# Performance work log

Hardware: AMD Instinct MI355X
Metric: run time of the kernel (lower is better)

## Reference

```python
import jax, jax.numpy as jnp
import numpy as np

DELTA = 5.0          # weight on positive BCE term
R = 0.01             # hard-negative fraction
M, N = 4096, 16384   # batch rows, memory-bank size
NUM_HARD = int(R * (N - 1))  # int(r * neg_count); each row has exactly 1 positive


def setup_inputs() -> dict:
    key = jax.random.key(0)
    k1, k2 = jax.random.split(key)
    inputs = jax.random.normal(k1, (M, N), dtype=jnp.float32)
    targets = jax.random.randint(k2, (M,), 0, N)
    return {"inputs": inputs, "targets": targets}


def reference(inputs, targets):
    m, n = inputs.shape
    rows = jnp.arange(m)
    # positive logit per row (one-hot scatter => exactly one positive)
    pos = inputs[rows, targets]                          # [m]
    # BCE with logits, target=1: softplus(-x); mean over the single positive
    l_pos = jax.nn.softplus(-pos)                        # [m]
    # exclude positive from negatives by sinking it to -inf, then hard top-k
    neg_inf = jnp.finfo(inputs.dtype).min
    masked = inputs.at[rows, targets].set(neg_inf)       # [m, n]
    hard_neg, _ = jax.lax.top_k(masked, NUM_HARD)        # [m, NUM_HARD]
    # BCE with logits, target=0: softplus(x); mean over hard negatives
    l_neg = jnp.mean(jax.nn.softplus(hard_neg), axis=1)  # [m]
    return jnp.mean(DELTA * l_pos + l_neg)
```

## Files before the change

kernel.cpp:

```cpp
#include <hip/hip_runtime.h>
#include <stdint.h>

#define M_ROWS 4096
#define N_COLS 16384
#define K_HARD 163
#define DELTA_W 5.0f
#define CAP    1024
#define NB1    4096
#define NB2    1024
#define BLOCK  256

__device__ __forceinline__ uint32_t f2key(float x) {
    uint32_t u = __float_as_uint(x);
    return u ^ (((int32_t)u >> 31) | 0x80000000u);
}
__device__ __forceinline__ float key2f(uint32_t k) {
    uint32_t u = (k & 0x80000000u) ? (k & 0x7fffffffu) : ~k;
    return __uint_as_float(u);
}
__device__ __forceinline__ float softplus_f(float x) {
    return fmaxf(x, 0.0f) + log1pf(__expf(-fabsf(x)));
}

#define KEY_MIN 0xC0000000u

__device__ void pivot_scan(const uint32_t* hist, int nb, int K,
                           int* part, int* pivot, int* krem) {
    const int t = threadIdx.x;
    const int bpt = nb / BLOCK;
    const int base = t * bpt;
    int mypart = 0;
    for (int i = 0; i < bpt; ++i) mypart += (int)hist[base + i];
    part[t] = mypart;
    __syncthreads();
    for (int off = 1; off < BLOCK; off <<= 1) {
        int v = part[t];
        if (t + off < BLOCK) v += part[t + off];
        __syncthreads();
        part[t] = v;
        __syncthreads();
    }
    const int above = part[t] - mypart;
    if (above < K && above + mypart >= K) {
        int running = above;
        for (int b = base + bpt - 1; b >= base; --b) {
            int c = (int)hist[b];
            if (running < K && running + c >= K) { *pivot = b; *krem = K - running; }
            running += c;
        }
    }
    __syncthreads();
}

__global__ __launch_bounds__(BLOCK) void mmcl_kernel(
        const float* __restrict__ inputs,
        const int* __restrict__ targets,
        float* __restrict__ out) {
    __shared__ uint32_t s_hist[NB1];
    __shared__ uint32_t s_cand[CAP];
    __shared__ int s_part[BLOCK];
    __shared__ int s_ncand;
    __shared__ int s_found;
    __shared__ int s_pivot;
    __shared__ int s_krem;
    __shared__ float s_pos;
    __shared__ float s_wsum[BLOCK / 64];

    const int row = blockIdx.x;
    const int t = threadIdx.x;
    const int lane = t & 63;
    const float* rowp = inputs + (size_t)row * N_COLS;
    const int target = targets[row];

    for (int i = t; i < NB1; i += BLOCK) s_hist[i] = 0;
    if (t == 0) { s_ncand = 0; s_found = -1; s_pos = rowp[target]; }
    __syncthreads();

    const float4* rp4 = (const float4*)rowp;
#pragma unroll 4
    for (int it = 0; it < N_COLS / (BLOCK * 4); ++it) {
        const float4 v = rp4[it * BLOCK + t];
        const uint32_t k0 = f2key(v.x), k1 = f2key(v.y),
                       k2 = f2key(v.z), k3 = f2key(v.w);
        if (k0 >= KEY_MIN) { int i = atomicAdd(&s_ncand, 1); if (i < CAP) s_cand[i] = k0; }
        if (k1 >= KEY_MIN) { int i = atomicAdd(&s_ncand, 1); if (i < CAP) s_cand[i] = k1; }
        if (k2 >= KEY_MIN) { int i = atomicAdd(&s_ncand, 1); if (i < CAP) s_cand[i] = k2; }
        if (k3 >= KEY_MIN) { int i = atomicAdd(&s_ncand, 1); if (i < CAP) s_cand[i] = k3; }
    }
    __syncthreads();

    const int ncand_raw = s_ncand;
    const uint32_t tkey = f2key(s_pos);
    const bool no_ovf = (ncand_raw <= CAP);
    if (no_ovf && tkey >= KEY_MIN) {
        for (int i = t; i < ncand_raw; i += BLOCK)
            if (s_cand[i] == tkey) { atomicCAS(&s_found, -1, i); break; }
    }
    __syncthreads();
    if (t == 0 && s_found >= 0) {
        s_cand[s_found] = s_cand[ncand_raw - 1];
        s_ncand = ncand_raw - 1;
    }
    __syncthreads();
    const int ncand = s_ncand;
    const bool fast = no_ovf && (ncand >= K_HARD);

    float local = 0.0f;
    uint32_t T;
    int tie;

    if (fast) {
        for (int i = t; i < ncand; i += BLOCK)
            atomicAdd(&s_hist[s_cand[i] >> 20], 1u);
        __syncthreads();
        pivot_scan(s_hist, NB1, K_HARD, s_part, &s_pivot, &s_krem);
        const int p1 = s_pivot, k1r = s_krem;

        for (int i = t; i < NB2; i += BLOCK) s_hist[i] = 0;
        __syncthreads();
        for (int i = t; i < ncand; i += BLOCK) {
            const uint32_t k = s_cand[i];
            if ((int)(k >> 20) == p1) atomicAdd(&s_hist[(k >> 10) & 1023u], 1u);
        }
        __syncthreads();
        pivot_scan(s_hist, NB2, k1r, s_part, &s_pivot, &s_krem);
        const int p2 = s_pivot, k2r = s_krem;
        const uint32_t pref2 = ((uint32_t)p1 << 10) | (uint32_t)p2;

        for (int i = t; i < NB2; i += BLOCK) s_hist[i] = 0;
        __syncthreads();
        for (int i = t; i < ncand; i += BLOCK) {
            const uint32_t k = s_cand[i];
            if ((k >> 10) == pref2) atomicAdd(&s_hist[k & 1023u], 1u);
        }
        __syncthreads();
        pivot_scan(s_hist, NB2, k2r, s_part, &s_pivot, &s_krem);
        T = (pref2 << 10) | (uint32_t)s_pivot;
        tie = s_krem;

        for (int i = t; i < ncand; i += BLOCK) {
            const uint32_t k = s_cand[i];
            if (k > T) local += softplus_f(key2f(k));
        }
    } else {
        for (int i = t; i < NB1; i += BLOCK) s_hist[i] = 0;
        __syncthreads();
        for (int j = t; j < N_COLS; j += BLOCK) {
            if (j == target) continue;
            atomicAdd(&s_hist[f2key(rowp[j]) >> 20], 1u);
        }
        __syncthreads();
        pivot_scan(s_hist, NB1, K_HARD, s_part, &s_pivot, &s_krem);
        const int p1 = s_pivot, k1r = s_krem;

        for (int i = t; i < NB2; i += BLOCK) s_hist[i] = 0;
        __syncthreads();
        for (int j = t; j < N_COLS; j += BLOCK) {
            if (j == target) continue;
            const uint32_t k = f2key(rowp[j]);
            if ((int)(k >> 20) == p1) atomicAdd(&s_hist[(k >> 10) & 1023u], 1u);
        }
        __syncthreads();
        pivot_scan(s_hist, NB2, k1r, s_part, &s_pivot, &s_krem);
        const int p2 = s_pivot, k2r = s_krem;
        const uint32_t pref2 = ((uint32_t)p1 << 10) | (uint32_t)p2;

        for (int i = t; i < NB2; i += BLOCK) s_hist[i] = 0;
        __syncthreads();
        for (int j = t; j < N_COLS; j += BLOCK) {
            if (j == target) continue;
            const uint32_t k = f2key(rowp[j]);
            if ((k >> 10) == pref2) atomicAdd(&s_hist[k & 1023u], 1u);
        }
        __syncthreads();
        pivot_scan(s_hist, NB2, k2r, s_part, &s_pivot, &s_krem);
        T = (pref2 << 10) | (uint32_t)s_pivot;
        tie = s_krem;

        for (int j = t; j < N_COLS; j += BLOCK) {
            if (j == target) continue;
            const uint32_t k = f2key(rowp[j]);
            if (k > T) local += softplus_f(key2f(k));
        }
    }

    for (int off = 32; off > 0; off >>= 1) local += __shfl_down(local, off);
    if (lane == 0) s_wsum[t >> 6] = local;
    __syncthreads();
    if (t == 0) {
        float tot = 0.0f;
        for (int w = 0; w < BLOCK / 64; ++w) tot += s_wsum[w];
        tot += (float)tie * softplus_f(key2f(T));
        const float l_neg = tot / (float)K_HARD;
        const float l_pos = softplus_f(-s_pos);
        const float rowval = (DELTA_W * l_pos + l_neg) * (1.0f / (float)M_ROWS);
        atomicAdd(out, rowval);
    }
}

__global__ void mmcl_zero_out(float* out) { out[0] = 0.0f; }

extern "C" void kernel_launch(void* const* d_in, const int* in_sizes, int n_in,
                              void* d_out, int out_size, void* d_ws, size_t ws_size,
                              hipStream_t stream) {
    const float* inputs = (const float*)d_in[0];
    const int* targets = (const int*)d_in[1];
    float* out = (float*)d_out;
    mmcl_zero_out<<<1, 1, 0, stream>>>(out);
    mmcl_kernel<<<M_ROWS, BLOCK, 0, stream>>>(inputs, targets, out);
}
```

Measured before the change: 400.3 us.

## Process eight rows per 1024-thread block with wave-level candidate selection

Replaces the one-row-per-256-thread-block kernel with 1024-thread blocks that stream eight rows each. Candidates at or above a fixed threshold of 2.0 are compacted into per-wave shared segments with a ballot/shuffle prefix sum, which removes the shared-memory atomic counter. Each row's radix select then runs inside a single wave using shuffle-based scans with no block barriers. A deterministic two-kernel partial-sum reduction replaces the global atomicAdd and the zeroing kernel. The risk is that the fixed threshold and the 64-entry segment cap push rows into the slow single-wave full-row fallback more often, and only half the waves take part in the selection phase.

```diff
diff --git a/kernel.cpp b/kernel.cpp
--- a/kernel.cpp
+++ b/kernel.cpp
@@ -5,14 +5,17 @@
 #define N_COLS 16384
 #define K_HARD 163
 #define DELTA_W 5.0f
-#define CAP    1024
-#define NB1    4096
-#define NB2    1024
-#define BLOCK  256
+#define THREADS 1024
+#define NWAVES  16
+#define RPB     8
+#define GRID    (M_ROWS / RPB)
+#define THRESH  2.0f
+#define KEY_MIN 0xC0000000u
+#define SEGC    64
 
 __device__ __forceinline__ uint32_t f2key(float x) {
     uint32_t u = __float_as_uint(x);
-    return u ^ (((int32_t)u >> 31) | 0x80000000u);
+    return u ^ (uint32_t)(((int32_t)u >> 31) | 0x80000000u);
 }
 __device__ __forceinline__ float key2f(uint32_t k) {
     uint32_t u = (k & 0x80000000u) ? (k & 0x7fffffffu) : ~k;
@@ -22,183 +25,224 @@
     return fmaxf(x, 0.0f) + log1pf(__expf(-fabsf(x)));
 }
 
-#define KEY_MIN 0xC0000000u
-
-__device__ void pivot_scan(const uint32_t* hist, int nb, int K,
-                           int* part, int* pivot, int* krem) {
-    const int t = threadIdx.x;
-    const int bpt = nb / BLOCK;
-    const int base = t * bpt;
-    int mypart = 0;
-    for (int i = 0; i < bpt; ++i) mypart += (int)hist[base + i];
-    part[t] = mypart;
-    __syncthreads();
-    for (int off = 1; off < BLOCK; off <<= 1) {
-        int v = part[t];
-        if (t + off < BLOCK) v += part[t + off];
-        __syncthreads();
-        part[t] = v;
-        __syncthreads();
-    }
-    const int above = part[t] - mypart;
-    if (above < K && above + mypart >= K) {
-        int running = above;
-        for (int b = base + bpt - 1; b >= base; --b) {
-            int c = (int)hist[b];
-            if (running < K && running + c >= K) { *pivot = b; *krem = K - running; }
-            running += c;
-        }
-    }
-    __syncthreads();
-}
-
-__global__ __launch_bounds__(BLOCK) void mmcl_kernel(
+__device__ __forceinline__ void wscan1024(const uint32_t* h, int lane, int K,
+                                          int& pivot, int& krem) {
+    int c[16]; int S = 0;
+#pragma unroll
+    for (int q = 0; q < 16; ++q) { c[q] = (int)h[lane * 16 + q]; S += c[q]; }
+    int suf = S;
+    for (int off = 1; off < 64; off <<= 1) {
+        int y = __shfl_down(suf, off);
+        if (lane + off < 64) suf += y;
+    }
+    int run = suf - S;
+    int enc = 0;
+#pragma unroll
+    for (int b = 15; b >= 0; --b) {
+        const int cc = c[b];
+        if (run < K && run + cc >= K) enc = ((lane * 16 + b + 1) << 8) | (K - run);
+        run += cc;
+    }
+    for (int off = 1; off < 64; off <<= 1) enc = max(enc, __shfl_xor(enc, off));
+    pivot = (enc >> 8) - 1; krem = enc & 255;
+}
+
+__device__ float wave_fallback(const float4* row4, int tgt, uint32_t* hrow, int lane) {
+    uint32_t pref = 0; int K = K_HARD;
+    for (int pass = 0; pass < 3; ++pass) {
+        const int shift = 22 - 10 * pass;
+        for (int q = 0; q < 16; ++q) hrow[q * 64 + lane] = 0;
+        for (int s2 = 0; s2 < 64; ++s2) {
+            const float4 v = row4[s2 * 64 + lane];
+            const int j0 = (s2 * 64 + lane) * 4;
+            const float e[4] = {v.x, v.y, v.z, v.w};
+#pragma unroll
+            for (int q = 0; q < 4; ++q) {
+                if (j0 + q == tgt) continue;
+                const uint32_t k = f2key(e[q]);
+                if (pass == 0 || (k >> (shift + 10)) == pref)
+                    atomicAdd(&hrow[(k >> shift) & 1023u], 1u);
+            }
+        }
+        int pv, kr; wscan1024(hrow, lane, K, pv, kr);
+        pref = (pref << 10) | (uint32_t)pv; K = kr;
+    }
+    for (int q = 0; q < 16; ++q) hrow[q * 64 + lane] = 0;
+    for (int s2 = 0; s2 < 64; ++s2) {
+        const float4 v = row4[s2 * 64 + lane];
+        const int j0 = (s2 * 64 + lane) * 4;
+        const float e[4] = {v.x, v.y, v.z, v.w};
+#pragma unroll
+        for (int q = 0; q < 4; ++q) {
+            if (j0 + q == tgt) continue;
+            const uint32_t k = f2key(e[q]);
+            if ((k >> 2) == pref) atomicAdd(&hrow[k & 3u], 1u);
+        }
+    }
+    int piv = 0, tie = K;
+    { int run = 0;
+      for (int b2 = 3; b2 >= 0; --b2) {
+          const int cc = (int)hrow[b2];
+          if (run < K && run + cc >= K) { piv = b2; tie = K - run; }
+          run += cc;
+      } }
+    const uint32_t T = (pref << 2) | (uint32_t)piv;
+    float sum = 0.0f;
+    for (int s2 = 0; s2 < 64; ++s2) {
+        const float4 v = row4[s2 * 64 + lane];
+        const int j0 = (s2 * 64 + lane) * 4;
+        const float e[4] = {v.x, v.y, v.z, v.w};
+#pragma unroll
+        for (int q = 0; q < 4; ++q) {
+            if (j0 + q == tgt) continue;
+            const uint32_t k = f2key(e[q]);
+            if (k > T) sum += softplus_f(e[q]);
+        }
+    }
+    for (int off = 32; off; off >>= 1) sum += __shfl_down(sum, off);
+    if (lane == 0) sum += (float)tie * softplus_f(key2f(T));
+    return sum;
+}
+
+__global__ __launch_bounds__(THREADS, 8) void mmcl_main(
         const float* __restrict__ inputs,
         const int* __restrict__ targets,
-        float* __restrict__ out) {
-    __shared__ uint32_t s_hist[NB1];
-    __shared__ uint32_t s_cand[CAP];
-    __shared__ int s_part[BLOCK];
-    __shared__ int s_ncand;
-    __shared__ int s_found;
-    __shared__ int s_pivot;
-    __shared__ int s_krem;
-    __shared__ float s_pos;
-    __shared__ float s_wsum[BLOCK / 64];
-
-    const int row = blockIdx.x;
+        float* __restrict__ partial) {
+    __shared__ uint32_t s_seg[NWAVES][RPB][SEGC];
+    __shared__ uint32_t s_hist[RPB][1024];
+    __shared__ int s_cnt[NWAVES][RPB];
+
+    const int b = blockIdx.x;
     const int t = threadIdx.x;
     const int lane = t & 63;
-    const float* rowp = inputs + (size_t)row * N_COLS;
-    const int target = targets[row];
-
-    for (int i = t; i < NB1; i += BLOCK) s_hist[i] = 0;
-    if (t == 0) { s_ncand = 0; s_found = -1; s_pos = rowp[target]; }
+    const int w = t >> 6;
+    const float4* in4 = (const float4*)inputs;
+    const int gbase = b * (RPB * 4096);
+
+    for (int r = 0; r < RPB; ++r) {
+        int wcount = 0;
+#pragma unroll
+        for (int ii = 0; ii < 4; ++ii) {
+            const float4 v = in4[gbase + (r * 4 + ii) * 1024 + t];
+            const float e[4] = {v.x, v.y, v.z, v.w};
+            const int n = (v.x >= THRESH) + (v.y >= THRESH) +
+                          (v.z >= THRESH) + (v.w >= THRESH);
+            int inc = n;
+            for (int off = 1; off < 64; off <<= 1) {
+                int y = __shfl_up(inc, off);
+                if (lane >= off) inc += y;
+            }
+            int base = wcount + inc - n;
+            int j = 0;
+#pragma unroll
+            for (int q = 0; q < 4; ++q) {
+                if (e[q] >= THRESH) {
+                    const int d = base + j;
+                    if (d < SEGC) s_seg[w][r][d] = f2key(e[q]);
+                    ++j;
+                }
+            }
+            wcount += __shfl(inc, 63);
+        }
+        if (lane == 0) s_cnt[w][r] = wcount;
+    }
     __syncthreads();
 
-    const float4* rp4 = (const float4*)rowp;
-#pragma unroll 4
-    for (int it = 0; it < N_COLS / (BLOCK * 4); ++it) {
-        const float4 v = rp4[it * BLOCK + t];
-        const uint32_t k0 = f2key(v.x), k1 = f2key(v.y),
-                       k2 = f2key(v.z), k3 = f2key(v.w);
-        if (k0 >= KEY_MIN) { int i = atomicAdd(&s_ncand, 1); if (i < CAP) s_cand[i] = k0; }
-        if (k1 >= KEY_MIN) { int i = atomicAdd(&s_ncand, 1); if (i < CAP) s_cand[i] = k1; }
-        if (k2 >= KEY_MIN) { int i = atomicAdd(&s_ncand, 1); if (i < CAP) s_cand[i] = k2; }
-        if (k3 >= KEY_MIN) { int i = atomicAdd(&s_ncand, 1); if (i < CAP) s_cand[i] = k3; }
-    }
+    if (w < RPB) {
+        const int r = w;
+        const int grow = b * RPB + r;
+        const int tgt = targets[grow];
+        const float pos = inputs[(size_t)grow * N_COLS + tgt];
+        const uint32_t tkey = f2key(pos);
+        const float4* row4 = (const float4*)(inputs + (size_t)grow * N_COLS);
+        uint32_t* hrow = &s_hist[r][0];
+
+        bool fb = false;
+        for (int s = 0; s < NWAVES; ++s) fb |= ((int)s_cnt[s][r] > SEGC);
+
+        if (!fb && pos >= THRESH) {
+            bool removed = false;
+            for (int s = 0; s < NWAVES && !removed; ++s) {
+                const int cc = (int)s_cnt[s][r];
+                const uint32_t k = (lane < cc) ? s_seg[s][r][lane] : (tkey + 1u);
+                const unsigned long long m = __ballot(lane < cc && k == tkey);
+                if (m) {
+                    const int f = __ffsll(m) - 1;
+                    if (lane == 0) {
+                        s_seg[s][r][f] = s_seg[s][r][cc - 1];
+                        s_cnt[s][r] = cc - 1;
+                    }
+                    removed = true;
+                }
+            }
+        }
+        int ncand = 0;
+        for (int s = 0; s < NWAVES; ++s) ncand += (int)s_cnt[s][r];
+        if (ncand < K_HARD) fb = true;
+
+        float sum;
+        if (!fb) {
+            for (int q = 0; q < 16; ++q) hrow[q * 64 + lane] = 0;
+            for (int s = 0; s < NWAVES; ++s) {
+                const int cc = (int)s_cnt[s][r];
+                if (lane < cc)
+                    atomicAdd(&hrow[(s_seg[s][r][lane] - KEY_MIN) >> 20], 1u);
+            }
+            int p1, k1; wscan1024(hrow, lane, K_HARD, p1, k1);
+            for (int q = 0; q < 16; ++q) hrow[q * 64 + lane] = 0;
+            for (int s = 0; s < NWAVES; ++s) {
+                const int cc = (int)s_cnt[s][r];
+                if (lane < cc) {
+                    const uint32_t d = s_seg[s][r][lane] - KEY_MIN;
+                    if ((int)(d >> 20) == p1) atomicAdd(&hrow[(d >> 10) & 1023u], 1u);
+                }
+            }
+            int p2, k2; wscan1024(hrow, lane, k1, p2, k2);
+            const uint32_t pref2 = ((uint32_t)p1 << 10) | (uint32_t)p2;
+            for (int q = 0; q < 16; ++q) hrow[q * 64 + lane] = 0;
+            for (int s = 0; s < NWAVES; ++s) {
+                const int cc = (int)s_cnt[s][r];
+                if (lane < cc) {
+                    const uint32_t d = s_seg[s][r][lane] - KEY_MIN;
+                    if ((d >> 10) == pref2) atomicAdd(&hrow[d & 1023u], 1u);
+                }
+            }
+            int p3, k3; wscan1024(hrow, lane, k2, p3, k3);
+            const uint32_t T = KEY_MIN +
+                (((uint32_t)p1 << 20) | ((uint32_t)p2 << 10) | (uint32_t)p3);
+            sum = 0.0f;
+            for (int s = 0; s < NWAVES; ++s) {
+                const int cc = (int)s_cnt[s][r];
+                if (lane < cc) {
+                    const uint32_t k = s_seg[s][r][lane];
+                    if (k > T) sum += softplus_f(key2f(k));
+                }
+            }
+            for (int off = 32; off; off >>= 1) sum += __shfl_down(sum, off);
+            if (lane == 0) sum += (float)k3 * softplus_f(key2f(T));
+        } else {
+            sum = wave_fallback(row4, tgt, hrow, lane);
+        }
+
+        if (lane == 0) {
+            const float l_neg = sum / (float)K_HARD;
+            partial[grow] = DELTA_W * softplus_f(-pos) + l_neg;
+        }
+    }
+}
+
+__global__ __launch_bounds__(256) void mmcl_reduce(
+        const float* __restrict__ partial, float* __restrict__ out) {
+    __shared__ float s_fw[4];
+    const int t = threadIdx.x;
+    float local = 0.0f;
+    for (int i = t; i < M_ROWS; i += 256) local += partial[i];
+    for (int off = 32; off; off >>= 1) local += __shfl_down(local, off);
+    if ((t & 63) == 0) s_fw[t >> 6] = local;
     __syncthreads();
-
-    const int ncand_raw = s_ncand;
-    const uint32_t tkey = f2key(s_pos);
-    const bool no_ovf = (ncand_raw <= CAP);
-    if (no_ovf && tkey >= KEY_MIN) {
-        for (int i = t; i < ncand_raw; i += BLOCK)
-            if (s_cand[i] == tkey) { atomicCAS(&s_found, -1, i); break; }
-    }
-    __syncthreads();
-    if (t == 0 && s_found >= 0) {
-        s_cand[s_found] = s_cand[ncand_raw - 1];
-        s_ncand = ncand_raw - 1;
-    }
-    __syncthreads();
-    const int ncand = s_ncand;
-    const bool fast = no_ovf && (ncand >= K_HARD);
-
-    float local = 0.0f;
-    uint32_t T;
-    int tie;
-
-    if (fast) {
-        for (int i = t; i < ncand; i += BLOCK)
-            atomicAdd(&s_hist[s_cand[i] >> 20], 1u);
-        __syncthreads();
-        pivot_scan(s_hist, NB1, K_HARD, s_part, &s_pivot, &s_krem);
-        const int p1 = s_pivot, k1r = s_krem;
-
-        for (int i = t; i < NB2; i += BLOCK) s_hist[i] = 0;
-        __syncthreads();
-        for (int i = t; i < ncand; i += BLOCK) {
-            const uint32_t k = s_cand[i];
-            if ((int)(k >> 20) == p1) atomicAdd(&s_hist[(k >> 10) & 1023u], 1u);
-        }
-        __syncthreads();
-        pivot_scan(s_hist, NB2, k1r, s_part, &s_pivot, &s_krem);
-        const int p2 = s_pivot, k2r = s_krem;
-        const uint32_t pref2 = ((uint32_t)p1 << 10) | (uint32_t)p2;
-
-        for (int i = t; i < NB2; i += BLOCK) s_hist[i] = 0;
-        __syncthreads();
-        for (int i = t; i < ncand; i += BLOCK) {
-            const uint32_t k = s_cand[i];
-            if ((k >> 10) == pref2) atomicAdd(&s_hist[k & 1023u], 1u);
-        }
-        __syncthreads();
-        pivot_scan(s_hist, NB2, k2r, s_part, &s_pivot, &s_krem);
-        T = (pref2 << 10) | (uint32_t)s_pivot;
-        tie = s_krem;
-
-        for (int i = t; i < ncand; i += BLOCK) {
-            const uint32_t k = s_cand[i];
-            if (k > T) local += softplus_f(key2f(k));
-        }
-    } else {
-        for (int i = t; i < NB1; i += BLOCK) s_hist[i] = 0;
-        __syncthreads();
-        for (int j = t; j < N_COLS; j += BLOCK) {
-            if (j == target) continue;
-            atomicAdd(&s_hist[f2key(rowp[j]) >> 20], 1u);
-        }
-        __syncthreads();
-        pivot_scan(s_hist, NB1, K_HARD, s_part, &s_pivot, &s_krem);
-        const int p1 = s_pivot, k1r = s_krem;
-
-        for (int i = t; i < NB2; i += BLOCK) s_hist[i] = 0;
-        __syncthreads();
-        for (int j = t; j < N_COLS; j += BLOCK) {
-            if (j == target) continue;
-            const uint32_t k = f2key(rowp[j]);
-            if ((int)(k >> 20) == p1) atomicAdd(&s_hist[(k >> 10) & 1023u], 1u);
-        }
-        __syncthreads();
-        pivot_scan(s_hist, NB2, k1r, s_part, &s_pivot, &s_krem);
-        const int p2 = s_pivot, k2r = s_krem;
-        const uint32_t pref2 = ((uint32_t)p1 << 10) | (uint32_t)p2;
-
-        for (int i = t; i < NB2; i += BLOCK) s_hist[i] = 0;
-        __syncthreads();
-        for (int j = t; j < N_COLS; j += BLOCK) {
-            if (j == target) continue;
-            const uint32_t k = f2key(rowp[j]);
-            if ((k >> 10) == pref2) atomicAdd(&s_hist[k & 1023u], 1u);
-        }
-        __syncthreads();
-        pivot_scan(s_hist, NB2, k2r, s_part, &s_pivot, &s_krem);
-        T = (pref2 << 10) | (uint32_t)s_pivot;
-        tie = s_krem;
-
-        for (int j = t; j < N_COLS; j += BLOCK) {
-            if (j == target) continue;
-            const uint32_t k = f2key(rowp[j]);
-            if (k > T) local += softplus_f(key2f(k));
-        }
-    }
-
-    for (int off = 32; off > 0; off >>= 1) local += __shfl_down(local, off);
-    if (lane == 0) s_wsum[t >> 6] = local;
-    __syncthreads();
-    if (t == 0) {
-        float tot = 0.0f;
-        for (int w = 0; w < BLOCK / 64; ++w) tot += s_wsum[w];
-        tot += (float)tie * softplus_f(key2f(T));
-        const float l_neg = tot / (float)K_HARD;
-        const float l_pos = softplus_f(-s_pos);
-        const float rowval = (DELTA_W * l_pos + l_neg) * (1.0f / (float)M_ROWS);
-        atomicAdd(out, rowval);
-    }
-}
-
-__global__ void mmcl_zero_out(float* out) { out[0] = 0.0f; }
+    if (t == 0)
+        out[0] = (s_fw[0] + s_fw[1] + s_fw[2] + s_fw[3]) * (1.0f / (float)M_ROWS);
+}
 
 extern "C" void kernel_launch(void* const* d_in, const int* in_sizes, int n_in,
                               void* d_out, int out_size, void* d_ws, size_t ws_size,
@@ -206,6 +250,7 @@
     const float* inputs = (const float*)d_in[0];
     const int* targets = (const int*)d_in[1];
     float* out = (float*)d_out;
-    mmcl_zero_out<<<1, 1, 0, stream>>>(out);
-    mmcl_kernel<<<M_ROWS, BLOCK, 0, stream>>>(inputs, targets, out);
-}
+    float* partial = (float*)d_ws;
+    mmcl_main<<<GRID, THREADS, 0, stream>>>(inputs, targets, partial);
+    mmcl_reduce<<<1, 256, 0, stream>>>(partial, out);
+}
```

New measurement: 385.0 us. -3.8%, faster.
